# Kernel tuning notes

Measured on AMD Instinct MI355X. Metric: run time of the kernel, lower is better.

The kernel has to match this reference:

```python
import jax, jax.numpy as jnp
import numpy as np


def setup_inputs() -> dict:
    key = jax.random.key(0)
    ks = jax.random.split(key, 7)
    N, D, H1, H2, M = 16384, 2048, 512, 32, 2048
    return {
        "x": jax.random.normal(ks[0], (N, D), dtype=jnp.float32),
        "W1": jax.random.normal(ks[1], (H1, D), dtype=jnp.float32) * (1.0 / np.sqrt(D)),
        "b1": jax.random.normal(ks[2], (H1,), dtype=jnp.float32) * 0.01,
        "W2": jax.random.normal(ks[3], (H2, H1), dtype=jnp.float32) * (1.0 / np.sqrt(H1)),
        "b2": jax.random.normal(ks[4], (H2,), dtype=jnp.float32) * 0.01,
        "a_memory": jax.random.normal(ks[5], (M, H2), dtype=jnp.float32),
        "n_memory": jax.random.normal(ks[6], (M, H2), dtype=jnp.float32),
    }


def reference(x, W1, b1, W2, b2, a_memory, n_memory):
    # MLP per forward(): linear -> relu -> (dropout p=0) -> linear -> (dropout p=0)
    h = jax.nn.relu(x @ W1.T + b1)          # [N, 512]
    feat = h @ W2.T + b2                     # [N, 32] (no ReLU in forward path)
    inv_d = 1.0 / feat.shape[1]
    # caption_score(mem, f) = max_j mean(mem_j * f) = max_j (mem_j . f) / 32
    a_score = jnp.max(feat @ a_memory.T, axis=1) * inv_d  # [N]
    n_score = jnp.max(feat @ n_memory.T, axis=1) * inv_d  # [N]
    return jax.nn.sigmoid(a_score - n_score)
```

## Files before the change

### kernel.cpp

```cpp
#include <hip/hip_runtime.h>
#include <hip/hip_bf16.h>

typedef __attribute__((ext_vector_type(8))) __bf16 bf16x8;
typedef __attribute__((ext_vector_type(4))) float f32x4;

#define NROWS 16384
#define DIM   2048
#define NH1   512
#define NH2   32
#define MMEM  2048
#define NT    (DIM / 32)

#define W1O ((size_t)0)
#define W2O ((size_t)2097152)
#define AMO ((size_t)2129920)
#define NMO ((size_t)2260992)
#define HO  ((size_t)2392064)

__device__ __forceinline__ f32x4 mfma16(bf16x8 a, bf16x8 b, f32x4 c) {
    return __builtin_amdgcn_mfma_f32_16x16x32_bf16(a, b, c, 0, 0, 0);
}

__device__ __forceinline__ void gload_lds16(const void* g, void* l) {
    __builtin_amdgcn_global_load_lds(
        (const __attribute__((address_space(1))) void*)g,
        (__attribute__((address_space(3))) void*)l, 16, 0, 0);
}

__device__ __forceinline__ bf16x8 cvt8(float4 a, float4 b) {
    bf16x8 o;
    o[0] = (__bf16)a.x; o[1] = (__bf16)a.y; o[2] = (__bf16)a.z; o[3] = (__bf16)a.w;
    o[4] = (__bf16)b.x; o[5] = (__bf16)b.y; o[6] = (__bf16)b.z; o[7] = (__bf16)b.w;
    return o;
}

struct bf4 { __bf16 a, b, c, d; };

__global__ void cvt_all_kernel(const float* __restrict__ w1f, __bf16* __restrict__ w1b,
                               const float* __restrict__ w2f, __bf16* __restrict__ w2b,
                               const float* __restrict__ amf, __bf16* __restrict__ amb,
                               const float* __restrict__ nmf, __bf16* __restrict__ nmb) {
    const int g = blockIdx.x * blockDim.x + threadIdx.x;
    const int T = gridDim.x * blockDim.x;
    for (int i = g; i < (NH1 * DIM) / 4; i += T) {
        const float4 v = *reinterpret_cast<const float4*>(w1f + i * 4);
        *reinterpret_cast<bf4*>(w1b + i * 4) = { (__bf16)v.x, (__bf16)v.y, (__bf16)v.z, (__bf16)v.w };
    }
    for (int i = g; i < (NH2 * NH1) / 4; i += T) {
        const float4 v = *reinterpret_cast<const float4*>(w2f + i * 4);
        *reinterpret_cast<bf4*>(w2b + i * 4) = { (__bf16)v.x, (__bf16)v.y, (__bf16)v.z, (__bf16)v.w };
    }
    for (int i = g; i < (MMEM * NH2) / 4; i += T) {
        const float4 v = *reinterpret_cast<const float4*>(amf + i * 4);
        *reinterpret_cast<bf4*>(amb + i * 4) = { (__bf16)v.x, (__bf16)v.y, (__bf16)v.z, (__bf16)v.w };
    }
    for (int i = g; i < (MMEM * NH2) / 4; i += T) {
        const float4 v = *reinterpret_cast<const float4*>(nmf + i * 4);
        *reinterpret_cast<bf4*>(nmb + i * 4) = { (__bf16)v.x, (__bf16)v.y, (__bf16)v.z, (__bf16)v.w };
    }
}

__global__ __launch_bounds__(256) void gemm1_kernel(
    const float*  __restrict__ Xf,
    const __bf16* __restrict__ W1,
    const float*  __restrict__ b1,
    __bf16* __restrict__ Hout)
{
    __shared__ __bf16 bufA[2][64 * 32];
    __shared__ __bf16 bufB[2][128 * 32];
    const int tid  = threadIdx.x;
    const int lane = tid & 63;
    const int wave = tid >> 6;
    const int b = blockIdx.x;
    const int orig = (b & 7) * 128 + (b >> 3);
    const int bn = orig & 3;
    const int bm = orig >> 2;
    const size_t brow = (size_t)bm * 64;
    const int bcol = bn * 128;
    const int wr = wave >> 1, wc = wave & 1;

    f32x4 acc[2][4];
#pragma unroll
    for (int m = 0; m < 2; ++m)
#pragma unroll
        for (int n = 0; n < 4; ++n) acc[m][n] = (f32x4){0.f, 0.f, 0.f, 0.f};

    const int sArow = tid >> 2;
    const int sAcol = (tid & 3) * 8;
    const float* aSrc = Xf + (brow + sArow) * (size_t)DIM + sAcol;
    const int aOff = sArow * 32 + sAcol;

    const char* bSrcBase = (const char*)(W1 + (size_t)(bcol + (tid >> 2)) * DIM) + (tid & 3) * 16;
    const int bDstOff = wave * 1024;

    const int l15 = lane & 15;
    const int kc  = lane >> 4;
    const int rA = wr * 32 + l15;
    const int rB = wc * 64 + l15;

    {
        float4 ta0 = *(const float4*)(aSrc);
        float4 ta1 = *(const float4*)(aSrc + 4);
        *(bf16x8*)(bufA[0] + aOff) = cvt8(ta0, ta1);
        gload_lds16(bSrcBase, (char*)bufB[0] + bDstOff);
        gload_lds16(bSrcBase + (size_t)64 * DIM * 2, (char*)bufB[0] + bDstOff + 4096);
    }
    __builtin_amdgcn_sched_barrier(0);
    float4 pa0 = *(const float4*)(aSrc + 32);
    float4 pa1 = *(const float4*)(aSrc + 36);
    asm volatile("s_waitcnt vmcnt(2) lgkmcnt(0)" ::: "memory");
    __builtin_amdgcn_s_barrier();

    for (int t = 0; t < NT - 1; ++t) {
        const int cur = t & 1;
        const __bf16* Acur = bufA[cur];
        const __bf16* Bcur = bufB[cur];

        const char* bS = bSrcBase + (size_t)(t + 1) * 64;
        gload_lds16(bS, (char*)bufB[cur ^ 1] + bDstOff);
        gload_lds16(bS + (size_t)64 * DIM * 2, (char*)bufB[cur ^ 1] + bDstOff + 4096);
        __builtin_amdgcn_sched_barrier(0);

        const int tq = (t + 2 < NT) ? (t + 2) : 0;
        const float* qs = aSrc + (size_t)tq * 32;
        float4 qa0 = *(const float4*)(qs);
        float4 qa1 = *(const float4*)(qs + 4);

        *(bf16x8*)(bufA[cur ^ 1] + aOff) = cvt8(pa0, pa1);

        bf16x8 av[2], bv[4];
#pragma unroll
        for (int m = 0; m < 2; ++m) av[m] = *(const bf16x8*)(Acur + (rA + m * 16) * 32 + kc * 8);
#pragma unroll
        for (int n = 0; n < 4; ++n) bv[n] = *(const bf16x8*)(Bcur + (rB + n * 16) * 32 + kc * 8);
#pragma unroll
        for (int m = 0; m < 2; ++m)
#pragma unroll
            for (int n = 0; n < 4; ++n)
                acc[m][n] = mfma16(av[m], bv[n], acc[m][n]);

        asm volatile("s_waitcnt vmcnt(2) lgkmcnt(0)" ::: "memory");
        __builtin_amdgcn_s_barrier();
        pa0 = qa0; pa1 = qa1;
    }

    {
        const int cur = (NT - 1) & 1;
        const __bf16* Acur = bufA[cur];
        const __bf16* Bcur = bufB[cur];
        bf16x8 av[2], bv[4];
#pragma unroll
        for (int m = 0; m < 2; ++m) av[m] = *(const bf16x8*)(Acur + (rA + m * 16) * 32 + kc * 8);
#pragma unroll
        for (int n = 0; n < 4; ++n) bv[n] = *(const bf16x8*)(Bcur + (rB + n * 16) * 32 + kc * 8);
#pragma unroll
        for (int m = 0; m < 2; ++m)
#pragma unroll
            for (int n = 0; n < 4; ++n)
                acc[m][n] = mfma16(av[m], bv[n], acc[m][n]);
    }

#pragma unroll
    for (int n = 0; n < 4; ++n) {
        const int gcol = bcol + wc * 64 + n * 16 + l15;
        const float bias = b1[gcol];
#pragma unroll
        for (int m = 0; m < 2; ++m) {
            const size_t grow0 = brow + wr * 32 + m * 16 + kc * 4;
#pragma unroll
            for (int r = 0; r < 4; ++r) {
                float v = acc[m][n][r] + bias;
                v = v > 0.f ? v : 0.f;
                Hout[(grow0 + r) * NH1 + gcol] = (__bf16)v;
            }
        }
    }
}

__global__ __launch_bounds__(512) void tail_kernel(
    const __bf16* __restrict__ Hin,
    const __bf16* __restrict__ W2b,
    const float*  __restrict__ b2,
    const __bf16* __restrict__ Am,
    const __bf16* __restrict__ Nm,
    float* __restrict__ out)
{
    __shared__ __bf16 featLds[64 * 32];
    __shared__ float aMaxLds[2][64];
    __shared__ float nMaxLds[2][64];
    const int tid  = threadIdx.x;
    const int lane = tid & 63;
    const int wave = tid >> 6;
    const int rowBase = blockIdx.x * 64;
    const int l15 = lane & 15;
    const int kc  = lane >> 4;
    const int rgrp  = (wave & 3) * 16;
    const int jHalf = wave >> 2;

    if (wave < 4) {
        f32x4 acc0 = {0.f,0.f,0.f,0.f}, acc1 = {0.f,0.f,0.f,0.f};
        const size_t hrow = (size_t)(rowBase + rgrp + l15) * NH1;
#pragma unroll
        for (int kk = 0; kk < 16; ++kk) {
            bf16x8 a  = *(const bf16x8*)(Hin + hrow + kk * 32 + kc * 8);
            bf16x8 w0 = *(const bf16x8*)(W2b + (size_t)l15 * NH1 + kk * 32 + kc * 8);
            bf16x8 w1 = *(const bf16x8*)(W2b + (size_t)(16 + l15) * NH1 + kk * 32 + kc * 8);
            acc0 = mfma16(a, w0, acc0);
            acc1 = mfma16(a, w1, acc1);
        }
        const float bias0 = b2[l15], bias1 = b2[16 + l15];
#pragma unroll
        for (int r = 0; r < 4; ++r) {
            const int lr = rgrp + kc * 4 + r;
            featLds[lr * 32 + l15]      = (__bf16)(acc0[r] + bias0);
            featLds[lr * 32 + 16 + l15] = (__bf16)(acc1[r] + bias1);
        }
    }
    __syncthreads();

    const bf16x8 af = *(const bf16x8*)&featLds[(rgrp + l15) * 32 + kc * 8];

    float rmaxA[4], rmaxN[4];
#pragma unroll
    for (int r = 0; r < 4; ++r) { rmaxA[r] = -1e30f; rmaxN[r] = -1e30f; }
    const f32x4 zero = {0.f,0.f,0.f,0.f};
    const int jBase = jHalf * (MMEM / 2);
#pragma unroll 2
    for (int jt = 0; jt < (MMEM / 2) / 16; jt += 4) {
        bf16x8 ba[4], bb[4];
#pragma unroll
        for (int u = 0; u < 4; ++u) {
            const size_t off = (size_t)(jBase + (jt + u) * 16 + l15) * NH2 + kc * 8;
            ba[u] = *(const bf16x8*)(Am + off);
            bb[u] = *(const bf16x8*)(Nm + off);
        }
#pragma unroll
        for (int u = 0; u < 4; ++u) {
            f32x4 sa = mfma16(af, ba[u], zero);
            f32x4 sn = mfma16(af, bb[u], zero);
#pragma unroll
            for (int r = 0; r < 4; ++r) {
                rmaxA[r] = fmaxf(rmaxA[r], sa[r]);
                rmaxN[r] = fmaxf(rmaxN[r], sn[r]);
            }
        }
    }
#pragma unroll
    for (int off = 1; off < 16; off <<= 1) {
#pragma unroll
        for (int r = 0; r < 4; ++r) {
            rmaxA[r] = fmaxf(rmaxA[r], __shfl_xor(rmaxA[r], off, 64));
            rmaxN[r] = fmaxf(rmaxN[r], __shfl_xor(rmaxN[r], off, 64));
        }
    }
    if (l15 == 0) {
#pragma unroll
        for (int r = 0; r < 4; ++r) {
            const int row = rgrp + kc * 4 + r;
            aMaxLds[jHalf][row] = rmaxA[r];
            nMaxLds[jHalf][row] = rmaxN[r];
        }
    }
    __syncthreads();
    if (tid < 64) {
        const float ma = fmaxf(aMaxLds[0][tid], aMaxLds[1][tid]);
        const float mn = fmaxf(nMaxLds[0][tid], nMaxLds[1][tid]);
        const float d = (ma - mn) * (1.0f / 32.0f);
        out[rowBase + tid] = 1.0f / (1.0f + __expf(-d));
    }
}

extern "C" void kernel_launch(void* const* d_in, const int* in_sizes, int n_in,
                              void* d_out, int out_size, void* d_ws, size_t ws_size,
                              hipStream_t stream) {
    (void)in_sizes; (void)n_in; (void)out_size; (void)ws_size;
    const float* x  = (const float*)d_in[0];
    const float* W1 = (const float*)d_in[1];
    const float* b1 = (const float*)d_in[2];
    const float* W2 = (const float*)d_in[3];
    const float* b2 = (const float*)d_in[4];
    const float* am = (const float*)d_in[5];
    const float* nm = (const float*)d_in[6];
    float* out = (float*)d_out;
    char* ws = (char*)d_ws;
    __bf16* w1b = (__bf16*)(ws + W1O);
    __bf16* w2b = (__bf16*)(ws + W2O);
    __bf16* amb = (__bf16*)(ws + AMO);
    __bf16* nmb = (__bf16*)(ws + NMO);
    __bf16* hb  = (__bf16*)(ws + HO);

    cvt_all_kernel<<<dim3(512), dim3(256), 0, stream>>>(W1, w1b, W2, w2b, am, amb, nm, nmb);
    gemm1_kernel<<<dim3((NROWS / 64) * (NH1 / 128)), dim3(256), 0, stream>>>(x, w1b, b1, hb);
    tail_kernel<<<dim3(NROWS / 64), dim3(512), 0, stream>>>(hb, w2b, b2, amb, nmb, out);
}
```

Before: 92.51 us.

## Enlarge gemm1 tile to 128x128 with BK=64 and XOR-swizzled LDS

```diff
diff --git a/kernel.cpp b/kernel.cpp
--- a/kernel.cpp
+++ b/kernel.cpp
@@ -9,7 +9,8 @@
 #define NH1   512
 #define NH2   32
 #define MMEM  2048
-#define NT    (DIM / 32)
+#define BK    64
+#define NT2   (DIM / BK)
 
 #define W1O ((size_t)0)
 #define W2O ((size_t)2097152)
@@ -27,10 +28,10 @@
         (__attribute__((address_space(3))) void*)l, 16, 0, 0);
 }
 
-__device__ __forceinline__ bf16x8 cvt8(float4 a, float4 b) {
+__device__ __forceinline__ bf16x8 cvt8(f32x4 a, f32x4 b) {
     bf16x8 o;
-    o[0] = (__bf16)a.x; o[1] = (__bf16)a.y; o[2] = (__bf16)a.z; o[3] = (__bf16)a.w;
-    o[4] = (__bf16)b.x; o[5] = (__bf16)b.y; o[6] = (__bf16)b.z; o[7] = (__bf16)b.w;
+    o[0] = (__bf16)a[0]; o[1] = (__bf16)a[1]; o[2] = (__bf16)a[2]; o[3] = (__bf16)a[3];
+    o[4] = (__bf16)b[0]; o[5] = (__bf16)b[1]; o[6] = (__bf16)b[2]; o[7] = (__bf16)b[3];
     return o;
 }
 
@@ -60,104 +61,155 @@
     }
 }
 
-__global__ __launch_bounds__(256) void gemm1_kernel(
+__global__ __launch_bounds__(256, 2) void gemm1_kernel(
     const float*  __restrict__ Xf,
     const __bf16* __restrict__ W1,
     const float*  __restrict__ b1,
     __bf16* __restrict__ Hout)
 {
-    __shared__ __bf16 bufA[2][64 * 32];
-    __shared__ __bf16 bufB[2][128 * 32];
+    __shared__ __bf16 bufA[2][128 * BK];
+    __shared__ __bf16 bufB[2][128 * BK];
     const int tid  = threadIdx.x;
     const int lane = tid & 63;
     const int wave = tid >> 6;
     const int b = blockIdx.x;
-    const int orig = (b & 7) * 128 + (b >> 3);
+    const int orig = (b & 7) * 64 + (b >> 3);
     const int bn = orig & 3;
     const int bm = orig >> 2;
-    const size_t brow = (size_t)bm * 64;
+    const size_t brow = (size_t)bm * 128;
     const int bcol = bn * 128;
     const int wr = wave >> 1, wc = wave & 1;
 
-    f32x4 acc[2][4];
-#pragma unroll
-    for (int m = 0; m < 2; ++m)
+    f32x4 acc[4][4];
+#pragma unroll
+    for (int m = 0; m < 4; ++m)
 #pragma unroll
         for (int n = 0; n < 4; ++n) acc[m][n] = (f32x4){0.f, 0.f, 0.f, 0.f};
 
-    const int sArow = tid >> 2;
-    const int sAcol = (tid & 3) * 8;
-    const float* aSrc = Xf + (brow + sArow) * (size_t)DIM + sAcol;
-    const int aOff = sArow * 32 + sAcol;
-
-    const char* bSrcBase = (const char*)(W1 + (size_t)(bcol + (tid >> 2)) * DIM) + (tid & 3) * 16;
-    const int bDstOff = wave * 1024;
+    const int aRow  = tid >> 1;
+    const int aHalf = tid & 1;
+    const float* aSrc = Xf + (brow + aRow) * (size_t)DIM + aHalf * 32;
+    int aOffB[4];
+#pragma unroll
+    for (int j = 0; j < 4; ++j)
+        aOffB[j] = aRow * 128 + (((aHalf * 4 + j) ^ (aRow & 7)) << 4);
+
+    const int bRowL  = wave * 8 + (lane >> 3);
+    const int bChunk = (lane & 7) ^ (lane >> 3);
+    const char* bSrcBase = (const char*)W1 + ((size_t)(bcol + bRowL) * DIM) * 2 + bChunk * 16;
+    const int bLdsOff = wave * 1024 + lane * 16;
 
     const int l15 = lane & 15;
     const int kc  = lane >> 4;
-    const int rA = wr * 32 + l15;
-    const int rB = wc * 64 + l15;
-
+    const int l7  = lane & 7;
+    const int rABase = wr * 64 + l15;
+    const int rBBase = wc * 64 + l15;
+
+    f32x4 pa[8];
     {
-        float4 ta0 = *(const float4*)(aSrc);
-        float4 ta1 = *(const float4*)(aSrc + 4);
-        *(bf16x8*)(bufA[0] + aOff) = cvt8(ta0, ta1);
-        gload_lds16(bSrcBase, (char*)bufB[0] + bDstOff);
-        gload_lds16(bSrcBase + (size_t)64 * DIM * 2, (char*)bufB[0] + bDstOff + 4096);
-    }
-    __builtin_amdgcn_sched_barrier(0);
-    float4 pa0 = *(const float4*)(aSrc + 32);
-    float4 pa1 = *(const float4*)(aSrc + 36);
-    asm volatile("s_waitcnt vmcnt(2) lgkmcnt(0)" ::: "memory");
+        f32x4 ta[8];
+#pragma unroll
+        for (int j = 0; j < 4; ++j) {
+            ta[2 * j]     = *(const f32x4*)(aSrc + j * 8);
+            ta[2 * j + 1] = *(const f32x4*)(aSrc + j * 8 + 4);
+        }
+#pragma unroll
+        for (int q = 0; q < 4; ++q)
+            gload_lds16(bSrcBase + (size_t)q * 32 * DIM * 2,
+                        (char*)bufB[0] + q * 4096 + bLdsOff);
+        __builtin_amdgcn_sched_barrier(0);
+#pragma unroll
+        for (int j = 0; j < 4; ++j)
+            *(bf16x8*)((char*)bufA[0] + aOffB[j]) = cvt8(ta[2 * j], ta[2 * j + 1]);
+        __builtin_amdgcn_sched_barrier(0);
+#pragma unroll
+        for (int j = 0; j < 4; ++j) {
+            pa[2 * j]     = *(const f32x4*)(aSrc + BK + j * 8);
+            pa[2 * j + 1] = *(const f32x4*)(aSrc + BK + j * 8 + 4);
+        }
+        __builtin_amdgcn_sched_barrier(0);
+    }
+    asm volatile("s_waitcnt vmcnt(8) lgkmcnt(0)" ::: "memory");
     __builtin_amdgcn_s_barrier();
 
-    for (int t = 0; t < NT - 1; ++t) {
+    for (int t = 0; t < NT2 - 1; ++t) {
         const int cur = t & 1;
         const __bf16* Acur = bufA[cur];
         const __bf16* Bcur = bufB[cur];
-
-        const char* bS = bSrcBase + (size_t)(t + 1) * 64;
-        gload_lds16(bS, (char*)bufB[cur ^ 1] + bDstOff);
-        gload_lds16(bS + (size_t)64 * DIM * 2, (char*)bufB[cur ^ 1] + bDstOff + 4096);
-        __builtin_amdgcn_sched_barrier(0);
-
-        const int tq = (t + 2 < NT) ? (t + 2) : 0;
-        const float* qs = aSrc + (size_t)tq * 32;
-        float4 qa0 = *(const float4*)(qs);
-        float4 qa1 = *(const float4*)(qs + 4);
-
-        *(bf16x8*)(bufA[cur ^ 1] + aOff) = cvt8(pa0, pa1);
-
-        bf16x8 av[2], bv[4];
-#pragma unroll
-        for (int m = 0; m < 2; ++m) av[m] = *(const bf16x8*)(Acur + (rA + m * 16) * 32 + kc * 8);
-#pragma unroll
-        for (int n = 0; n < 4; ++n) bv[n] = *(const bf16x8*)(Bcur + (rB + n * 16) * 32 + kc * 8);
-#pragma unroll
-        for (int m = 0; m < 2; ++m)
+        char* Anxt = (char*)bufA[cur ^ 1];
+        char* Bnxt = (char*)bufB[cur ^ 1];
+
+        {
+            const char* bs = bSrcBase + (size_t)(t + 1) * BK * 2;
+#pragma unroll
+            for (int q = 0; q < 4; ++q)
+                gload_lds16(bs + (size_t)q * 32 * DIM * 2, Bnxt + q * 4096 + bLdsOff);
+        }
+        __builtin_amdgcn_sched_barrier(0);
+
+#pragma unroll
+        for (int j = 0; j < 4; ++j)
+            *(bf16x8*)(Anxt + aOffB[j]) = cvt8(pa[2 * j], pa[2 * j + 1]);
+        __builtin_amdgcn_sched_barrier(0);
+
+        f32x4 qa[8];
+        {
+            const int tq = (t + 2 < NT2) ? (t + 2) : 0;
+            const float* qs = aSrc + (size_t)tq * BK;
+#pragma unroll
+            for (int j = 0; j < 4; ++j) {
+                qa[2 * j]     = *(const f32x4*)(qs + j * 8);
+                qa[2 * j + 1] = *(const f32x4*)(qs + j * 8 + 4);
+            }
+        }
+        __builtin_amdgcn_sched_barrier(0);
+
+#pragma unroll
+        for (int kk = 0; kk < 2; ++kk) {
+            const int c = kk * 4 + kc;
+            const int slot = (c ^ l7) << 4;
+            bf16x8 av[4], bv[4];
+#pragma unroll
+            for (int m = 0; m < 4; ++m)
+                av[m] = *(const bf16x8*)((const char*)Acur + (rABase + m * 16) * 128 + slot);
 #pragma unroll
             for (int n = 0; n < 4; ++n)
-                acc[m][n] = mfma16(av[m], bv[n], acc[m][n]);
-
-        asm volatile("s_waitcnt vmcnt(2) lgkmcnt(0)" ::: "memory");
+                bv[n] = *(const bf16x8*)((const char*)Bcur + (rBBase + n * 16) * 128 + slot);
+#pragma unroll
+            for (int m = 0; m < 4; ++m)
+#pragma unroll
+                for (int n = 0; n < 4; ++n)
+                    acc[m][n] = mfma16(av[m], bv[n], acc[m][n]);
+        }
+
+        asm volatile("s_waitcnt vmcnt(8) lgkmcnt(0)" ::: "memory");
         __builtin_amdgcn_s_barrier();
-        pa0 = qa0; pa1 = qa1;
+
+#pragma unroll
+        for (int j = 0; j < 8; ++j) pa[j] = qa[j];
     }
 
     {
-        const int cur = (NT - 1) & 1;
+        const int cur = (NT2 - 1) & 1;
         const __bf16* Acur = bufA[cur];
         const __bf16* Bcur = bufB[cur];
-        bf16x8 av[2], bv[4];
-#pragma unroll
-        for (int m = 0; m < 2; ++m) av[m] = *(const bf16x8*)(Acur + (rA + m * 16) * 32 + kc * 8);
-#pragma unroll
-        for (int n = 0; n < 4; ++n) bv[n] = *(const bf16x8*)(Bcur + (rB + n * 16) * 32 + kc * 8);
-#pragma unroll
-        for (int m = 0; m < 2; ++m)
+#pragma unroll
+        for (int kk = 0; kk < 2; ++kk) {
+            const int c = kk * 4 + kc;
+            const int slot = (c ^ l7) << 4;
+            bf16x8 av[4], bv[4];
+#pragma unroll
+            for (int m = 0; m < 4; ++m)
+                av[m] = *(const bf16x8*)((const char*)Acur + (rABase + m * 16) * 128 + slot);
 #pragma unroll
             for (int n = 0; n < 4; ++n)
-                acc[m][n] = mfma16(av[m], bv[n], acc[m][n]);
+                bv[n] = *(const bf16x8*)((const char*)Bcur + (rBBase + n * 16) * 128 + slot);
+#pragma unroll
+            for (int m = 0; m < 4; ++m)
+#pragma unroll
+                for (int n = 0; n < 4; ++n)
+                    acc[m][n] = mfma16(av[m], bv[n], acc[m][n]);
+        }
     }
 
 #pragma unroll
@@ -165,8 +217,8 @@
         const int gcol = bcol + wc * 64 + n * 16 + l15;
         const float bias = b1[gcol];
 #pragma unroll
-        for (int m = 0; m < 2; ++m) {
-            const size_t grow0 = brow + wr * 32 + m * 16 + kc * 4;
+        for (int m = 0; m < 4; ++m) {
+            const size_t grow0 = brow + wr * 64 + m * 16 + kc * 4;
 #pragma unroll
             for (int r = 0; r < 4; ++r) {
                 float v = acc[m][n][r] + bias;
@@ -290,6 +342,6 @@
     __bf16* hb  = (__bf16*)(ws + HO);
 
     cvt_all_kernel<<<dim3(512), dim3(256), 0, stream>>>(W1, w1b, W2, w2b, am, amb, nm, nmb);
-    gemm1_kernel<<<dim3((NROWS / 64) * (NH1 / 128)), dim3(256), 0, stream>>>(x, w1b, b1, hb);
+    gemm1_kernel<<<dim3((NROWS / 128) * (NH1 / 128)), dim3(256), 0, stream>>>(x, w1b, b1, hb);
     tail_kernel<<<dim3(NROWS / 64), dim3(512), 0, stream>>>(hb, w2b, b2, amb, nmb, out);
 }
```

Result: slower. 108.1 us (+16.9%).

## Rework gemm1 into 128x128 tiles with triple-buffered direct-to-LDS fp32 A loads

Applied to the files above, without the earlier changes.

```diff
diff --git a/kernel.cpp b/kernel.cpp
--- a/kernel.cpp
+++ b/kernel.cpp
@@ -9,7 +9,8 @@
 #define NH1   512
 #define NH2   32
 #define MMEM  2048
-#define NT    (DIM / 32)
+#define BK    32
+#define NT    (DIM / BK)
 
 #define W1O ((size_t)0)
 #define W2O ((size_t)2097152)
@@ -27,10 +28,10 @@
         (__attribute__((address_space(3))) void*)l, 16, 0, 0);
 }
 
-__device__ __forceinline__ bf16x8 cvt8(float4 a, float4 b) {
+__device__ __forceinline__ bf16x8 cvt8(f32x4 a, f32x4 b) {
     bf16x8 o;
-    o[0] = (__bf16)a.x; o[1] = (__bf16)a.y; o[2] = (__bf16)a.z; o[3] = (__bf16)a.w;
-    o[4] = (__bf16)b.x; o[5] = (__bf16)b.y; o[6] = (__bf16)b.z; o[7] = (__bf16)b.w;
+    o[0] = (__bf16)a[0]; o[1] = (__bf16)a[1]; o[2] = (__bf16)a[2]; o[3] = (__bf16)a[3];
+    o[4] = (__bf16)b[0]; o[5] = (__bf16)b[1]; o[6] = (__bf16)b[2]; o[7] = (__bf16)b[3];
     return o;
 }
 
@@ -60,113 +61,117 @@
     }
 }
 
-__global__ __launch_bounds__(256) void gemm1_kernel(
+__global__ __launch_bounds__(256, 2) void gemm1_kernel(
     const float*  __restrict__ Xf,
     const __bf16* __restrict__ W1,
     const float*  __restrict__ b1,
     __bf16* __restrict__ Hout)
 {
-    __shared__ __bf16 bufA[2][64 * 32];
-    __shared__ __bf16 bufB[2][128 * 32];
+    __shared__ float  As[3][128 * BK];
+    __shared__ __bf16 Bs[3][128 * BK];
     const int tid  = threadIdx.x;
     const int lane = tid & 63;
     const int wave = tid >> 6;
     const int b = blockIdx.x;
-    const int orig = (b & 7) * 128 + (b >> 3);
+    const int orig = (b & 7) * 64 + (b >> 3);
     const int bn = orig & 3;
     const int bm = orig >> 2;
-    const size_t brow = (size_t)bm * 64;
+    const size_t brow = (size_t)bm * 128;
     const int bcol = bn * 128;
     const int wr = wave >> 1, wc = wave & 1;
 
-    f32x4 acc[2][4];
-#pragma unroll
-    for (int m = 0; m < 2; ++m)
+    f32x4 acc[4][4];
+#pragma unroll
+    for (int m = 0; m < 4; ++m)
 #pragma unroll
         for (int n = 0; n < 4; ++n) acc[m][n] = (f32x4){0.f, 0.f, 0.f, 0.f};
 
-    const int sArow = tid >> 2;
-    const int sAcol = (tid & 3) * 8;
-    const float* aSrc = Xf + (brow + sArow) * (size_t)DIM + sAcol;
-    const int aOff = sArow * 32 + sAcol;
-
-    const char* bSrcBase = (const char*)(W1 + (size_t)(bcol + (tid >> 2)) * DIM) + (tid & 3) * 16;
-    const int bDstOff = wave * 1024;
+    const int aRowT = tid >> 3;
+    const int cA    = (tid & 7) ^ (aRowT & 7);
+    const float* aSrcBase = Xf + (brow + aRowT) * (size_t)DIM + cA * 4;
+    const int bRowT = tid >> 2;
+    const int cB    = (tid & 3) ^ (bRowT & 3);
+    const __bf16* bSrcBase = W1 + (size_t)(bcol + bRowT) * DIM + cB * 8;
+
+#define STAGE(T, BI)                                                          \
+    {                                                                         \
+        const int k0_ = (T) * BK;                                             \
+        _Pragma("unroll")                                                     \
+        for (int q = 0; q < 4; ++q)                                           \
+            gload_lds16(aSrcBase + (size_t)q * 32 * DIM + k0_,                \
+                        (char*)As[BI] + q * 4096 + tid * 16);                 \
+        _Pragma("unroll")                                                     \
+        for (int q = 0; q < 2; ++q)                                           \
+            gload_lds16(bSrcBase + (size_t)q * 64 * DIM + k0_,                \
+                        (char*)Bs[BI] + q * 4096 + tid * 16);                 \
+    }
 
     const int l15 = lane & 15;
     const int kc  = lane >> 4;
-    const int rA = wr * 32 + l15;
-    const int rB = wc * 64 + l15;
-
+    const int l7  = lane & 7;
+    const int rABase = wr * 64 + l15;
+    const int rBBase = wc * 64 + l15;
+    const int aSlot0 = ((2 * kc)     ^ l7) << 4;
+    const int aSlot1 = ((2 * kc + 1) ^ l7) << 4;
+    const int bSlot  = (kc ^ (lane & 3)) << 4;
+
+#define COMPUTE(BI)                                                           \
+    {                                                                         \
+        const char* Ac = (const char*)As[BI];                                 \
+        const char* Bc = (const char*)Bs[BI];                                 \
+        bf16x8 av[4], bv[4];                                                  \
+        _Pragma("unroll")                                                     \
+        for (int m = 0; m < 4; ++m) {                                         \
+            const int rowB = (rABase + m * 16) * 128;                         \
+            f32x4 lo = *(const f32x4*)(Ac + rowB + aSlot0);                   \
+            f32x4 hi = *(const f32x4*)(Ac + rowB + aSlot1);                   \
+            av[m] = cvt8(lo, hi);                                             \
+        }                                                                     \
+        _Pragma("unroll")                                                     \
+        for (int n = 0; n < 4; ++n)                                           \
+            bv[n] = *(const bf16x8*)(Bc + (rBBase + n * 16) * 64 + bSlot);    \
+        __builtin_amdgcn_s_setprio(1);                                        \
+        _Pragma("unroll")                                                     \
+        for (int m = 0; m < 4; ++m)                                           \
+            _Pragma("unroll")                                                 \
+            for (int n = 0; n < 4; ++n)                                       \
+                acc[m][n] = mfma16(av[m], bv[n], acc[m][n]);                  \
+        __builtin_amdgcn_s_setprio(0);                                        \
+    }
+
+    STAGE(0, 0);
+    STAGE(1, 1);
+
+    for (int t = 0; t < NT - 2; ++t) {
+        const int bi = t % 3;
+        asm volatile("s_waitcnt vmcnt(6)" ::: "memory");
+        __builtin_amdgcn_s_barrier();
+        __builtin_amdgcn_sched_barrier(0);
+        COMPUTE(bi);
+        __builtin_amdgcn_sched_barrier(0);
+        const int bnx = (t + 2) % 3;
+        STAGE(t + 2, bnx);
+    }
     {
-        float4 ta0 = *(const float4*)(aSrc);
-        float4 ta1 = *(const float4*)(aSrc + 4);
-        *(bf16x8*)(bufA[0] + aOff) = cvt8(ta0, ta1);
-        gload_lds16(bSrcBase, (char*)bufB[0] + bDstOff);
-        gload_lds16(bSrcBase + (size_t)64 * DIM * 2, (char*)bufB[0] + bDstOff + 4096);
-    }
-    __builtin_amdgcn_sched_barrier(0);
-    float4 pa0 = *(const float4*)(aSrc + 32);
-    float4 pa1 = *(const float4*)(aSrc + 36);
-    asm volatile("s_waitcnt vmcnt(2) lgkmcnt(0)" ::: "memory");
-    __builtin_amdgcn_s_barrier();
-
-    for (int t = 0; t < NT - 1; ++t) {
-        const int cur = t & 1;
-        const __bf16* Acur = bufA[cur];
-        const __bf16* Bcur = bufB[cur];
-
-        const char* bS = bSrcBase + (size_t)(t + 1) * 64;
-        gload_lds16(bS, (char*)bufB[cur ^ 1] + bDstOff);
-        gload_lds16(bS + (size_t)64 * DIM * 2, (char*)bufB[cur ^ 1] + bDstOff + 4096);
+        asm volatile("s_waitcnt vmcnt(6)" ::: "memory");
+        __builtin_amdgcn_s_barrier();
         __builtin_amdgcn_sched_barrier(0);
-
-        const int tq = (t + 2 < NT) ? (t + 2) : 0;
-        const float* qs = aSrc + (size_t)tq * 32;
-        float4 qa0 = *(const float4*)(qs);
-        float4 qa1 = *(const float4*)(qs + 4);
-
-        *(bf16x8*)(bufA[cur ^ 1] + aOff) = cvt8(pa0, pa1);
-
-        bf16x8 av[2], bv[4];
-#pragma unroll
-        for (int m = 0; m < 2; ++m) av[m] = *(const bf16x8*)(Acur + (rA + m * 16) * 32 + kc * 8);
-#pragma unroll
-        for (int n = 0; n < 4; ++n) bv[n] = *(const bf16x8*)(Bcur + (rB + n * 16) * 32 + kc * 8);
-#pragma unroll
-        for (int m = 0; m < 2; ++m)
-#pragma unroll
-            for (int n = 0; n < 4; ++n)
-                acc[m][n] = mfma16(av[m], bv[n], acc[m][n]);
-
-        asm volatile("s_waitcnt vmcnt(2) lgkmcnt(0)" ::: "memory");
+        COMPUTE((NT - 2) % 3);
+        asm volatile("s_waitcnt vmcnt(0)" ::: "memory");
         __builtin_amdgcn_s_barrier();
-        pa0 = qa0; pa1 = qa1;
-    }
-
-    {
-        const int cur = (NT - 1) & 1;
-        const __bf16* Acur = bufA[cur];
-        const __bf16* Bcur = bufB[cur];
-        bf16x8 av[2], bv[4];
-#pragma unroll
-        for (int m = 0; m < 2; ++m) av[m] = *(const bf16x8*)(Acur + (rA + m * 16) * 32 + kc * 8);
-#pragma unroll
-        for (int n = 0; n < 4; ++n) bv[n] = *(const bf16x8*)(Bcur + (rB + n * 16) * 32 + kc * 8);
-#pragma unroll
-        for (int m = 0; m < 2; ++m)
-#pragma unroll
-            for (int n = 0; n < 4; ++n)
-                acc[m][n] = mfma16(av[m], bv[n], acc[m][n]);
-    }
+        __builtin_amdgcn_sched_barrier(0);
+        COMPUTE((NT - 1) % 3);
+    }
+#undef STAGE
+#undef COMPUTE
 
 #pragma unroll
     for (int n = 0; n < 4; ++n) {
         const int gcol = bcol + wc * 64 + n * 16 + l15;
         const float bias = b1[gcol];
 #pragma unroll
-        for (int m = 0; m < 2; ++m) {
-            const size_t grow0 = brow + wr * 32 + m * 16 + kc * 4;
+        for (int m = 0; m < 4; ++m) {
+            const size_t grow0 = brow + wr * 64 + m * 16 + kc * 4;
 #pragma unroll
             for (int r = 0; r < 4; ++r) {
                 float v = acc[m][n][r] + bias;
@@ -290,6 +295,6 @@
     __bf16* hb  = (__bf16*)(ws + HO);
 
     cvt_all_kernel<<<dim3(512), dim3(256), 0, stream>>>(W1, w1b, W2, w2b, am, amb, nm, nmb);
-    gemm1_kernel<<<dim3((NROWS / 64) * (NH1 / 128)), dim3(256), 0, stream>>>(x, w1b, b1, hb);
+    gemm1_kernel<<<dim3((NROWS / 128) * (NH1 / 128)), dim3(256), 0, stream>>>(x, w1b, b1, hb);
     tail_kernel<<<dim3(NROWS / 64), dim3(512), 0, stream>>>(hb, w2b, b2, amb, nmb, out);
 }
```

New measurement: 81.67 us. 11.7% less time.
